# Kernel optimization log

Hardware: AMD Instinct MI355X
Metric: run time of the kernel (lower is better)

## Reference

```python
import jax, jax.numpy as jnp
import numpy as np

N_SVC = 100000
N_EP = 100000
E = 300000
D = 128
H = 128


def _sage(x_src, x_dst, edge_index, Wl, bl, Wr, n_dst):
    """PyG SAGEConv default: mean neighbor aggr, lin_l(aggr) + lin_r(x_dst)."""
    src, dst = edge_index[0], edge_index[1]
    msg = x_src[src]                                        # [E, D] gather
    sums = jax.ops.segment_sum(msg, dst, num_segments=n_dst)  # [n_dst, D]
    cnt = jax.ops.segment_sum(jnp.ones((msg.shape[0], 1), msg.dtype), dst,
                              num_segments=n_dst)             # [n_dst, 1]
    mean = sums / jnp.maximum(cnt, 1.0)
    return mean @ Wl.T + bl + x_dst @ Wr.T                  # [n_dst, H]


def setup_inputs() -> dict:
    key = jax.random.key(0)
    ks = jax.random.split(key, 16)
    scale = 1.0 / np.sqrt(D)
    inp = {
        "x_service": jax.random.normal(ks[0], (N_SVC, D), jnp.float32),
        "x_endpoint": jax.random.normal(ks[1], (N_EP, D), jnp.float32),
        "ei_calls": jax.random.randint(ks[2], (2, E), 0, N_SVC),   # svc -> svc
        "ei_has": jax.random.randint(ks[3], (2, E), 0, N_SVC),     # svc -> ep (dst < N_EP too)
        "ei_belongs": jax.random.randint(ks[4], (2, E), 0, N_EP),  # ep -> svc
        "Wl_calls": jax.random.normal(ks[5], (H, D), jnp.float32) * scale,
        "bl_calls": jnp.zeros((H,), jnp.float32),
        "Wr_calls": jax.random.normal(ks[6], (H, D), jnp.float32) * scale,
        "Wl_has": jax.random.normal(ks[7], (H, D), jnp.float32) * scale,
        "bl_has": jnp.zeros((H,), jnp.float32),
        "Wr_has": jax.random.normal(ks[8], (H, D), jnp.float32) * scale,
        "Wl_belongs": jax.random.normal(ks[9], (H, D), jnp.float32) * scale,
        "bl_belongs": jnp.zeros((H,), jnp.float32),
        "Wr_belongs": jax.random.normal(ks[10], (H, D), jnp.float32) * scale,
    }
    return inp


def reference(x_service, x_endpoint, ei_calls, ei_has, ei_belongs,
              Wl_calls, bl_calls, Wr_calls,
              Wl_has, bl_has, Wr_has,
              Wl_belongs, bl_belongs, Wr_belongs):
    # edge type (service, calls, service) -> service output
    out_calls = _sage(x_service, x_service, ei_calls, Wl_calls, bl_calls, Wr_calls, N_SVC)
    # edge type (endpoint, belongs, service) -> service output
    out_belongs = _sage(x_endpoint, x_service, ei_belongs, Wl_belongs, bl_belongs, Wr_belongs, N_SVC)
    # edge type (service, has, endpoint) -> endpoint output
    out_has = _sage(x_service, x_endpoint, ei_has, Wl_has, bl_has, Wr_has, N_EP)
    # HeteroConv aggr='sum': sum per destination node type
    out_service = out_calls + out_belongs
    out_endpoint = out_has
    return out_service, out_endpoint
```

## Files before the change

### kernel.cpp

```cpp
#include <hip/hip_runtime.h>

#define DF 128
#define CAP 24

typedef __bf16 bf16x8 __attribute__((ext_vector_type(8)));
typedef float f32x4 __attribute__((ext_vector_type(4)));
typedef unsigned short ushort8v __attribute__((ext_vector_type(8)));

__device__ __forceinline__ unsigned short f2bf(float f) {
    union { float f; unsigned int u; } v; v.f = f;
    unsigned int r = v.u + 0x7FFFu + ((v.u >> 16) & 1u);
    return (unsigned short)(r >> 16);
}
__device__ __forceinline__ float bf2f(unsigned short u) {
    union { unsigned int u; float f; } v; v.u = ((unsigned int)u) << 16;
    return v.f;
}

__global__ __launch_bounds__(256)
void prep_kernel(
                 const int* __restrict__ ei_calls, int E1,
                 const int* __restrict__ ei_belongs, int E2,
                 const int* __restrict__ ei_has, int E3,
                 int* __restrict__ cnt, int* __restrict__ slots,
                 const float* __restrict__ x_service,
                 const float* __restrict__ x_endpoint,
                 unsigned short* __restrict__ xb_svc,
                 unsigned short* __restrict__ xb_ep,
                 int n_svc, int n_ep,
                 const float* __restrict__ Wl_calls, const float* __restrict__ Wr_calls,
                 const float* __restrict__ Wl_belongs, const float* __restrict__ Wr_belongs,
                 const float* __restrict__ Wl_has, const float* __restrict__ Wr_has,
                 const float* __restrict__ bl_calls, const float* __restrict__ bl_belongs,
                 const float* __restrict__ bl_has,
                 unsigned short* __restrict__ Bp_svc, unsigned short* __restrict__ Bp_ep,
                 float* __restrict__ bias_svc, float* __restrict__ bias_ep,
                 int B_fill, int B_pack)
{
    int b = blockIdx.x;

    if (b < B_fill) {
        int e = b * 256 + threadIdx.x;
        int Etot = E1 + E2 + E3;
        if (e >= Etot) return;
        int s, d, base;
        if (e < E1)           { s = ei_calls[e]; d = ei_calls[E1 + e]; base = 0; }
        else if (e < E1 + E2) { int el = e - E1; s = ei_belongs[el]; d = ei_belongs[E2 + el]; base = n_svc; }
        else                  { int el = e - E1 - E2; s = ei_has[el]; d = ei_has[E3 + el]; base = 2 * n_svc; }
        int g = base + d;
        int pos = atomicAdd(cnt + g, 1);
        if (pos < CAP) slots[(size_t)g * CAP + pos] = s;
        return;
    }
    b -= B_fill;

    if (b < B_pack) {
        int t = b * 256 + threadIdx.x;
        const int SV = 12 * 8 * 64 * 8;
        const int EPN = 8 * 8 * 64 * 8;
        if (t < SV) {
            int j = t & 7, lane = (t >> 3) & 63, ct = (t >> 9) & 7, kt = t >> 12;
            int k = kt * 32 + (lane >> 4) * 8 + j;
            int n = ct * 16 + (lane & 15);
            float v;
            if (k < 128)       v = Wl_calls[n * DF + k];
            else if (k < 256)  v = Wl_belongs[n * DF + (k - 128)];
            else               v = Wr_calls[n * DF + (k - 256)] + Wr_belongs[n * DF + (k - 256)];
            Bp_svc[t] = f2bf(v);
        } else if (t < SV + EPN) {
            int t2 = t - SV;
            int j = t2 & 7, lane = (t2 >> 3) & 63, ct = (t2 >> 9) & 7, kt = t2 >> 12;
            int k = kt * 32 + (lane >> 4) * 8 + j;
            int n = ct * 16 + (lane & 15);
            float v = (k < 128) ? Wl_has[n * DF + k] : Wr_has[n * DF + (k - 128)];
            Bp_ep[t2] = f2bf(v);
        }
        if (t < 128) bias_svc[t] = bl_calls[t] + bl_belongs[t];
        else if (t < 256) bias_ep[t - 128] = bl_has[t - 128];
        return;
    }
    b -= B_pack;

    int tid = b * 256 + threadIdx.x;
    int node = tid >> 5;
    int c4 = (tid & 31) << 2;
    if (node < n_svc) {
        float4 v = *reinterpret_cast<const float4*>(x_service + (size_t)node * DF + c4);
        ushort4 o; o.x = f2bf(v.x); o.y = f2bf(v.y); o.z = f2bf(v.z); o.w = f2bf(v.w);
        *reinterpret_cast<ushort4*>(xb_svc + (size_t)node * DF + c4) = o;
    } else if (node < n_svc + n_ep) {
        int ne = node - n_svc;
        float4 v = *reinterpret_cast<const float4*>(x_endpoint + (size_t)ne * DF + c4);
        ushort4 o; o.x = f2bf(v.x); o.y = f2bf(v.y); o.z = f2bf(v.z); o.w = f2bf(v.w);
        *reinterpret_cast<ushort4*>(xb_ep + (size_t)ne * DF + c4) = o;
    }
}

template <int MODE>
__global__ __launch_bounds__(512, 4)
void fused_gemm(const unsigned short* __restrict__ xb_svc,
                const unsigned short* __restrict__ xb_ep,
                const int* __restrict__ cnt,
                const int* __restrict__ slots,
                const unsigned short* __restrict__ Bpack,
                const float* __restrict__ bias,
                float* __restrict__ out,
                int n_svc, int n_ep)
{
    constexpr int MK      = (MODE == 0) ? 256 : 128;
    constexpr int KSTEPS  = (MODE == 0) ? 12 : 8;
    constexpr int MKSTEPS = MK / 32;
    constexpr int NG      = (MODE == 0) ? 256 : 128;

    __shared__ unsigned short smean[128 * MK];

    const int M = (MODE == 0) ? n_svc : n_ep;
    const int row_base = blockIdx.x * 128;

#pragma unroll 1
    for (int it = 0; it < NG * 16 / 512; ++it) {
        int task   = it * 512 + threadIdx.x;
        int gl     = task >> 4;
        int lane16 = task & 15;
        int node   = gl & 127;
        int t      = gl >> 7;
        int chunk  = lane16 + t * 16;
        unsigned short* dst = smean + node * MK + ((chunk ^ (node & 7)) << 3);

        int gnode = row_base + node;
        float acc[8];
#pragma unroll
        for (int q = 0; q < 8; ++q) acc[q] = 0.f;
        int deg = 0;
        if (gnode < M) {
            int g;
            const unsigned short* src;
            if (MODE == 0) {
                g   = (t == 0) ? gnode : (n_svc + gnode);
                src = (t == 0) ? xb_svc : xb_ep;
            } else {
                g   = 2 * n_svc + gnode;
                src = xb_svc;
            }
            deg = cnt[g];
            if (deg > CAP) deg = CAP;
            const int* sp = slots + (size_t)g * CAP;
            int c8 = lane16 << 3;
            if (deg > 0 && deg <= 4) {
                int idx[4];
#pragma unroll
                for (int j = 0; j < 4; ++j) {
                    int ii = j; if (ii > deg - 1) ii = deg - 1;
                    idx[j] = sp[ii];
                }
                ushort8v v[4];
#pragma unroll
                for (int j = 0; j < 4; ++j)
                    v[j] = *reinterpret_cast<const ushort8v*>(
                        src + (size_t)idx[j] * DF + c8);
#pragma unroll
                for (int j = 0; j < 4; ++j) {
                    if (j < deg) {
#pragma unroll
                        for (int q = 0; q < 8; ++q) acc[q] += bf2f(v[j][q]);
                    }
                }
            } else if (deg > 4) {
                for (int i0 = 0; i0 < deg; i0 += 8) {
                    int idx[8];
#pragma unroll
                    for (int j = 0; j < 8; ++j) {
                        int ii = i0 + j;
                        if (ii > deg - 1) ii = deg - 1;
                        idx[j] = sp[ii];
                    }
                    ushort8v v[8];
#pragma unroll
                    for (int j = 0; j < 8; ++j)
                        v[j] = *reinterpret_cast<const ushort8v*>(
                            src + (size_t)idx[j] * DF + c8);
                    int nv = deg - i0;
#pragma unroll
                    for (int j = 0; j < 8; ++j) {
                        if (j < nv) {
#pragma unroll
                            for (int q = 0; q < 8; ++q) acc[q] += bf2f(v[j][q]);
                        }
                    }
                }
            }
        }
        float inv = 1.0f / (float)max(deg, 1);
        ushort8v o;
#pragma unroll
        for (int q = 0; q < 8; ++q) o[q] = f2bf(acc[q] * inv);
        *reinterpret_cast<ushort8v*>(dst) = o;
    }
    __syncthreads();

    const int lane = threadIdx.x & 63;
    const int wave = threadIdx.x >> 6;
    const int wr   = wave >> 1;
    const int wc   = wave & 1;
    const int quad = lane >> 4;
    const int lc   = lane & 15;
    const int m0l  = wr * 32 + lc;
    const int m1l  = m0l + 16;
    int m0 = row_base + m0l; if (m0 > M - 1) m0 = M - 1;
    int m1 = row_base + m1l; if (m1 > M - 1) m1 = M - 1;

    const unsigned short* xb_dst = (MODE == 0) ? xb_svc : xb_ep;
    const unsigned short* Xp0 = xb_dst + (size_t)m0 * DF + quad * 8;
    const unsigned short* Xp1 = xb_dst + (size_t)m1 * DF + quad * 8;
    const unsigned short* Bp  = Bpack + lane * 8 + wc * 4 * 512;

    f32x4 acc0[4], acc1[4];
#pragma unroll
    for (int ct = 0; ct < 4; ++ct) {
        acc0[ct] = (f32x4){0.f, 0.f, 0.f, 0.f};
        acc1[ct] = (f32x4){0.f, 0.f, 0.f, 0.f};
    }

#pragma unroll
    for (int kt = 0; kt < KSTEPS; ++kt) {
        bf16x8 af0, af1;
        if (kt < MKSTEPS) {
            int c = kt * 4 + quad;
            af0 = *reinterpret_cast<const bf16x8*>(
                smean + m0l * MK + ((c ^ (m0l & 7)) << 3));
            af1 = *reinterpret_cast<const bf16x8*>(
                smean + m1l * MK + ((c ^ (m1l & 7)) << 3));
        } else {
            af0 = *reinterpret_cast<const bf16x8*>(Xp0 + (kt - MKSTEPS) * 32);
            af1 = *reinterpret_cast<const bf16x8*>(Xp1 + (kt - MKSTEPS) * 32);
        }
        const unsigned short* bptr = Bp + (size_t)kt * 8 * 512;
#pragma unroll
        for (int ct = 0; ct < 4; ++ct) {
            bf16x8 bf = *reinterpret_cast<const bf16x8*>(bptr + ct * 512);
            acc0[ct] = __builtin_amdgcn_mfma_f32_16x16x32_bf16(af0, bf, acc0[ct], 0, 0, 0);
            acc1[ct] = __builtin_amdgcn_mfma_f32_16x16x32_bf16(af1, bf, acc1[ct], 0, 0, 0);
        }
    }

    float bc[4];
#pragma unroll
    for (int ct = 0; ct < 4; ++ct) bc[ct] = bias[(wc * 4 + ct) * 16 + lc];

    const int row0 = row_base + wr * 32;
#pragma unroll
    for (int half = 0; half < 2; ++half) {
        int orow0 = row0 + half * 16 + quad * 4;
        f32x4* accp = half ? acc1 : acc0;
#pragma unroll
        for (int r = 0; r < 4; ++r) {
            int orow = orow0 + r;
            if (orow < M) {
                float* op = out + (size_t)orow * DF + wc * 64 + lc;
#pragma unroll
                for (int ct = 0; ct < 4; ++ct) op[ct * 16] = accp[ct][r] + bc[ct];
            }
        }
    }
}

extern "C" void kernel_launch(void* const* d_in, const int* in_sizes, int n_in,
                              void* d_out, int out_size, void* d_ws, size_t ws_size,
                              hipStream_t stream)
{
    const float* x_service  = (const float*)d_in[0];
    const float* x_endpoint = (const float*)d_in[1];
    const int*   ei_calls   = (const int*)d_in[2];
    const int*   ei_has     = (const int*)d_in[3];
    const int*   ei_belongs = (const int*)d_in[4];
    const float* Wl_calls   = (const float*)d_in[5];
    const float* bl_calls   = (const float*)d_in[6];
    const float* Wr_calls   = (const float*)d_in[7];
    const float* Wl_has     = (const float*)d_in[8];
    const float* bl_has     = (const float*)d_in[9];
    const float* Wr_has     = (const float*)d_in[10];
    const float* Wl_belongs = (const float*)d_in[11];
    const float* bl_belongs = (const float*)d_in[12];
    const float* Wr_belongs = (const float*)d_in[13];

    const int n_svc = in_sizes[0] / DF;
    const int n_ep  = in_sizes[1] / DF;
    const int E1 = in_sizes[2] / 2;
    const int E3 = in_sizes[3] / 2;
    const int E2 = in_sizes[4] / 2;
    const int Etot = E1 + E2 + E3;
    const int NT = 2 * n_svc + n_ep;

    int* wsi = (int*)d_ws;
    size_t oi = 0;
    int* cnt   = wsi + oi; oi += NT;
    int* slots = wsi + oi; oi += (size_t)NT * CAP;
    oi = (oi + 3) & ~(size_t)3;

    unsigned short* wsu = (unsigned short*)(wsi + oi);
    size_t ou = 0;
    unsigned short* xb_svc = wsu + ou; ou += (size_t)n_svc * DF;
    unsigned short* xb_ep  = wsu + ou; ou += (size_t)n_ep * DF;
    unsigned short* Bp_svc = wsu + ou; ou += 12 * 8 * 64 * 8;
    unsigned short* Bp_ep  = wsu + ou; ou += 8 * 8 * 64 * 8;
    ou = (ou + 7) & ~(size_t)7;
    float* bias_svc = (float*)(wsu + ou);
    float* bias_ep  = bias_svc + DF;

    hipMemsetAsync(cnt, 0, (size_t)NT * sizeof(int), stream);

    const int B_fill = (Etot + 255) / 256;
    const int B_pack = (12 * 8 * 64 * 8 + 8 * 8 * 64 * 8 + 255) / 256;
    const int B_conv = (int)(((size_t)(n_svc + n_ep) * 32 + 255) / 256);

    prep_kernel<<<B_fill + B_pack + B_conv, 256, 0, stream>>>(
        ei_calls, E1, ei_belongs, E2, ei_has, E3, cnt, slots,
        x_service, x_endpoint, xb_svc, xb_ep, n_svc, n_ep,
        Wl_calls, Wr_calls, Wl_belongs, Wr_belongs, Wl_has, Wr_has,
        bl_calls, bl_belongs, bl_has, Bp_svc, Bp_ep, bias_svc, bias_ep,
        B_fill, B_pack);

    float* out_svc = (float*)d_out;
    float* out_ep  = out_svc + (size_t)n_svc * DF;

    fused_gemm<0><<<(n_svc + 127) / 128, 512, 0, stream>>>(
        xb_svc, xb_ep, cnt, slots, Bp_svc, bias_svc, out_svc, n_svc, n_ep);
    fused_gemm<1><<<(n_ep + 127) / 128, 512, 0, stream>>>(
        xb_svc, xb_ep, cnt, slots, Bp_ep, bias_ep, out_ep, n_svc, n_ep);
}
```

Before: 389.9 us.

## Halve rows per block and software-pipeline low-degree neighbor gathers

Each block now handles 64 rows instead of 128, and the 8 waves are rearranged as 2x4 so each wave computes 2 column tiles. The gather stage loads all degrees and the first four slot indices up front, then double-buffers the feature loads for the next task while accumulating the current one. Nodes with more than four neighbors go to a separate second loop. The goal is more loads in flight, more blocks for latency hiding, and less LDS per block, at the cost of more registers and twice as many blocks that each reload the B matrix.

```diff
diff --git a/kernel.cpp b/kernel.cpp
--- a/kernel.cpp
+++ b/kernel.cpp
@@ -110,98 +110,142 @@
     constexpr int MK      = (MODE == 0) ? 256 : 128;
     constexpr int KSTEPS  = (MODE == 0) ? 12 : 8;
     constexpr int MKSTEPS = MK / 32;
-    constexpr int NG      = (MODE == 0) ? 256 : 128;
-
-    __shared__ unsigned short smean[128 * MK];
+    constexpr int ROWS    = 64;
+    constexpr int NG      = (MODE == 0) ? 2 * ROWS : ROWS;
+    constexpr int NI      = NG * 16 / 512;
+
+    __shared__ unsigned short smean[ROWS * MK];
 
     const int M = (MODE == 0) ? n_svc : n_ep;
-    const int row_base = blockIdx.x * 128;
-
-#pragma unroll 1
-    for (int it = 0; it < NG * 16 / 512; ++it) {
-        int task   = it * 512 + threadIdx.x;
-        int gl     = task >> 4;
-        int lane16 = task & 15;
-        int node   = gl & 127;
-        int t      = gl >> 7;
-        int chunk  = lane16 + t * 16;
-        unsigned short* dst = smean + node * MK + ((chunk ^ (node & 7)) << 3);
-
+    const int row_base = blockIdx.x * ROWS;
+
+    const int lane16 = threadIdx.x & 15;
+    const int c8 = lane16 << 3;
+
+    int degA[NI];
+    int gA[NI];
+    const unsigned short* srcA[NI];
+    unsigned short* dstA[NI];
+
+#pragma unroll
+    for (int it = 0; it < NI; ++it) {
+        int gl   = (it * 512 + threadIdx.x) >> 4;
+        int node = gl & (ROWS - 1);
+        int t    = gl / ROWS;
+        int chunk = lane16 + t * 16;
+        dstA[it] = smean + node * MK + ((chunk ^ (node & 7)) << 3);
         int gnode = row_base + node;
+        int gn_c  = gnode < M ? gnode : M - 1;
+        int g;
+        if (MODE == 0) {
+            g = (t == 0) ? gn_c : (n_svc + gn_c);
+            srcA[it] = (t == 0) ? xb_svc : xb_ep;
+        } else {
+            g = 2 * n_svc + gn_c;
+            srcA[it] = xb_svc;
+        }
+        gA[it] = g;
+        int d = cnt[g];
+        if (gnode >= M) d = 0;
+        if (d > CAP) d = CAP;
+        degA[it] = d;
+    }
+
+    int4 s4[NI];
+#pragma unroll
+    for (int it = 0; it < NI; ++it)
+        s4[it] = *reinterpret_cast<const int4*>(slots + (size_t)gA[it] * CAP);
+
+    int idxA[NI][4];
+#pragma unroll
+    for (int it = 0; it < NI; ++it) {
+        int d = degA[it];
+        idxA[it][0] = (0 < d) ? s4[it].x : 0;
+        idxA[it][1] = (1 < d) ? s4[it].y : 0;
+        idxA[it][2] = (2 < d) ? s4[it].z : 0;
+        idxA[it][3] = (3 < d) ? s4[it].w : 0;
+    }
+
+    ushort8v vb0[4], vb1[4];
+#pragma unroll
+    for (int j = 0; j < 4; ++j)
+        vb0[j] = *reinterpret_cast<const ushort8v*>(
+            srcA[0] + (size_t)idxA[0][j] * DF + c8);
+
+#pragma unroll
+    for (int it = 0; it < NI; ++it) {
+        if (it + 1 < NI) {
+#pragma unroll
+            for (int j = 0; j < 4; ++j) {
+                const ushort8v* p = reinterpret_cast<const ushort8v*>(
+                    srcA[it + 1] + (size_t)idxA[it + 1][j] * DF + c8);
+                if ((it & 1) == 0) vb1[j] = *p; else vb0[j] = *p;
+            }
+        }
         float acc[8];
 #pragma unroll
         for (int q = 0; q < 8; ++q) acc[q] = 0.f;
-        int deg = 0;
-        if (gnode < M) {
-            int g;
-            const unsigned short* src;
-            if (MODE == 0) {
-                g   = (t == 0) ? gnode : (n_svc + gnode);
-                src = (t == 0) ? xb_svc : xb_ep;
-            } else {
-                g   = 2 * n_svc + gnode;
-                src = xb_svc;
+#pragma unroll
+        for (int j = 0; j < 4; ++j) {
+            if (j < degA[it]) {
+                ushort8v v = ((it & 1) == 0) ? vb0[j] : vb1[j];
+#pragma unroll
+                for (int q = 0; q < 8; ++q) acc[q] += bf2f(v[q]);
             }
-            deg = cnt[g];
-            if (deg > CAP) deg = CAP;
-            const int* sp = slots + (size_t)g * CAP;
-            int c8 = lane16 << 3;
-            if (deg > 0 && deg <= 4) {
-                int idx[4];
-#pragma unroll
-                for (int j = 0; j < 4; ++j) {
-                    int ii = j; if (ii > deg - 1) ii = deg - 1;
+        }
+        if (degA[it] <= 4) {
+            float inv = 1.0f / (float)max(degA[it], 1);
+            ushort8v o;
+#pragma unroll
+            for (int q = 0; q < 8; ++q) o[q] = f2bf(acc[q] * inv);
+            *reinterpret_cast<ushort8v*>(dstA[it]) = o;
+        }
+    }
+
+#pragma unroll
+    for (int it = 0; it < NI; ++it) {
+        int deg = degA[it];
+        if (deg > 4) {
+            const int* sp = slots + (size_t)gA[it] * CAP;
+            const unsigned short* src = srcA[it];
+            float acc[8];
+#pragma unroll
+            for (int q = 0; q < 8; ++q) acc[q] = 0.f;
+            for (int i0 = 0; i0 < deg; i0 += 8) {
+                int idx[8];
+#pragma unroll
+                for (int j = 0; j < 8; ++j) {
+                    int ii = i0 + j;
+                    if (ii > deg - 1) ii = deg - 1;
                     idx[j] = sp[ii];
                 }
-                ushort8v v[4];
-#pragma unroll
-                for (int j = 0; j < 4; ++j)
+                ushort8v v[8];
+#pragma unroll
+                for (int j = 0; j < 8; ++j)
                     v[j] = *reinterpret_cast<const ushort8v*>(
                         src + (size_t)idx[j] * DF + c8);
-#pragma unroll
-                for (int j = 0; j < 4; ++j) {
-                    if (j < deg) {
+                int nv = deg - i0;
+#pragma unroll
+                for (int j = 0; j < 8; ++j) {
+                    if (j < nv) {
 #pragma unroll
                         for (int q = 0; q < 8; ++q) acc[q] += bf2f(v[j][q]);
                     }
                 }
-            } else if (deg > 4) {
-                for (int i0 = 0; i0 < deg; i0 += 8) {
-                    int idx[8];
-#pragma unroll
-                    for (int j = 0; j < 8; ++j) {
-                        int ii = i0 + j;
-                        if (ii > deg - 1) ii = deg - 1;
-                        idx[j] = sp[ii];
-                    }
-                    ushort8v v[8];
-#pragma unroll
-                    for (int j = 0; j < 8; ++j)
-                        v[j] = *reinterpret_cast<const ushort8v*>(
-                            src + (size_t)idx[j] * DF + c8);
-                    int nv = deg - i0;
-#pragma unroll
-                    for (int j = 0; j < 8; ++j) {
-                        if (j < nv) {
-#pragma unroll
-                            for (int q = 0; q < 8; ++q) acc[q] += bf2f(v[j][q]);
-                        }
-                    }
-                }
             }
-        }
-        float inv = 1.0f / (float)max(deg, 1);
-        ushort8v o;
-#pragma unroll
-        for (int q = 0; q < 8; ++q) o[q] = f2bf(acc[q] * inv);
-        *reinterpret_cast<ushort8v*>(dst) = o;
+            float inv = 1.0f / (float)deg;
+            ushort8v o;
+#pragma unroll
+            for (int q = 0; q < 8; ++q) o[q] = f2bf(acc[q] * inv);
+            *reinterpret_cast<ushort8v*>(dstA[it]) = o;
+        }
     }
     __syncthreads();
 
     const int lane = threadIdx.x & 63;
     const int wave = threadIdx.x >> 6;
-    const int wr   = wave >> 1;
-    const int wc   = wave & 1;
+    const int wr   = wave >> 2;
+    const int wc   = wave & 3;
     const int quad = lane >> 4;
     const int lc   = lane & 15;
     const int m0l  = wr * 32 + lc;
@@ -212,11 +256,11 @@
     const unsigned short* xb_dst = (MODE == 0) ? xb_svc : xb_ep;
     const unsigned short* Xp0 = xb_dst + (size_t)m0 * DF + quad * 8;
     const unsigned short* Xp1 = xb_dst + (size_t)m1 * DF + quad * 8;
-    const unsigned short* Bp  = Bpack + lane * 8 + wc * 4 * 512;
-
-    f32x4 acc0[4], acc1[4];
-#pragma unroll
-    for (int ct = 0; ct < 4; ++ct) {
+    const unsigned short* Bp  = Bpack + lane * 8 + (wc * 2) * 512;
+
+    f32x4 acc0[2], acc1[2];
+#pragma unroll
+    for (int ct = 0; ct < 2; ++ct) {
         acc0[ct] = (f32x4){0.f, 0.f, 0.f, 0.f};
         acc1[ct] = (f32x4){0.f, 0.f, 0.f, 0.f};
     }
@@ -236,16 +280,16 @@
         }
         const unsigned short* bptr = Bp + (size_t)kt * 8 * 512;
 #pragma unroll
-        for (int ct = 0; ct < 4; ++ct) {
+        for (int ct = 0; ct < 2; ++ct) {
             bf16x8 bf = *reinterpret_cast<const bf16x8*>(bptr + ct * 512);
             acc0[ct] = __builtin_amdgcn_mfma_f32_16x16x32_bf16(af0, bf, acc0[ct], 0, 0, 0);
             acc1[ct] = __builtin_amdgcn_mfma_f32_16x16x32_bf16(af1, bf, acc1[ct], 0, 0, 0);
         }
     }
 
-    float bc[4];
-#pragma unroll
-    for (int ct = 0; ct < 4; ++ct) bc[ct] = bias[(wc * 4 + ct) * 16 + lc];
+    float bc[2];
+#pragma unroll
+    for (int ct = 0; ct < 2; ++ct) bc[ct] = bias[(wc * 2 + ct) * 16 + lc];
 
     const int row0 = row_base + wr * 32;
 #pragma unroll
@@ -256,9 +300,9 @@
         for (int r = 0; r < 4; ++r) {
             int orow = orow0 + r;
             if (orow < M) {
-                float* op = out + (size_t)orow * DF + wc * 64 + lc;
-#pragma unroll
-                for (int ct = 0; ct < 4; ++ct) op[ct * 16] = accp[ct][r] + bc[ct];
+                float* op = out + (size_t)orow * DF + wc * 32 + lc;
+#pragma unroll
+                for (int ct = 0; ct < 2; ++ct) op[ct * 16] = accp[ct][r] + bc[ct];
             }
         }
     }
@@ -323,8 +367,8 @@
     float* out_svc = (float*)d_out;
     float* out_ep  = out_svc + (size_t)n_svc * DF;
 
-    fused_gemm<0><<<(n_svc + 127) / 128, 512, 0, stream>>>(
+    fused_gemm<0><<<(n_svc + 63) / 64, 512, 0, stream>>>(
         xb_svc, xb_ep, cnt, slots, Bp_svc, bias_svc, out_svc, n_svc, n_ep);
-    fused_gemm<1><<<(n_ep + 127) / 128, 512, 0, stream>>>(
+    fused_gemm<1><<<(n_ep + 63) / 64, 512, 0, stream>>>(
         xb_svc, xb_ep, cnt, slots, Bp_ep, bias_ep, out_ep, n_svc, n_ep);
 }
```

Result: faster. 365.7 us (-6.2%).
